# Optimization experiments

Hardware: AMD Instinct MI355X
Metric: run time of the kernel (lower is better)

Reference implementation:

```python
import jax, jax.numpy as jnp
import numpy as np
from jax import lax

FEAT_STRIDE = 16
NMS_THRESH = 0.7
N_PRE = 6000   # test-mode n_test_pre_nms
N_POST = 300   # test-mode n_test_post_nms
MIN_SIZE = 16.0
SCALE = 1.0
RATIOS = (0.5, 1.0, 2.0)
ANCHOR_SCALES = (8, 16, 32)
BASE = 16
N_ANCHOR = len(RATIOS) * len(ANCHOR_SCALES)  # 9


def _anchor_base():
    py = px = BASE / 2.0
    ab = np.zeros((N_ANCHOR, 4), np.float32)
    for i, r in enumerate(RATIOS):
        for j, s in enumerate(ANCHOR_SCALES):
            h = BASE * s * np.sqrt(r)
            w = BASE * s * np.sqrt(1.0 / r)
            k = i * len(ANCHOR_SCALES) + j
            ab[k] = [py - h / 2.0, px - w / 2.0, py + h / 2.0, px + w / 2.0]
    return ab


def _anchors(hh, ww):
    # enumerate_shifted_anchor: (y1,x1,y2,x2) anchors for every feature cell
    ab = _anchor_base()
    sy = np.arange(0, hh * FEAT_STRIDE, FEAT_STRIDE)
    sx = np.arange(0, ww * FEAT_STRIDE, FEAT_STRIDE)
    SX, SY = np.meshgrid(sx, sy)
    shift = np.stack([SY.ravel(), SX.ravel(), SY.ravel(), SX.ravel()], 1)
    anc = (ab[None, :, :] + shift[:, None, :]).reshape(-1, 4).astype(np.float32)
    return jnp.asarray(anc)


def _iou(b):
    # b: [N,4] (y1,x1,y2,x2) -> [N,N] IoU
    y1, x1, y2, x2 = b[:, 0], b[:, 1], b[:, 2], b[:, 3]
    area = (y2 - y1) * (x2 - x1)
    ih = jnp.clip(jnp.minimum(y2[:, None], y2[None, :]) - jnp.maximum(y1[:, None], y1[None, :]), 0.0)
    iw = jnp.clip(jnp.minimum(x2[:, None], x2[None, :]) - jnp.maximum(x1[:, None], x1[None, :]), 0.0)
    inter = ih * iw
    return inter / (area[:, None] + area[None, :] - inter + 1e-9)


def _propose(loc, fg, anchor, img_h, img_w):
    # loc:[M,4] fg:[M] anchor:[M,4]  -> padded [N_POST,4] rois + valid mask
    ah = anchor[:, 2] - anchor[:, 0]
    aw = anchor[:, 3] - anchor[:, 1]
    acy = anchor[:, 0] + 0.5 * ah
    acx = anchor[:, 1] + 0.5 * aw
    cy = loc[:, 0] * ah + acy
    cx = loc[:, 1] * aw + acx
    h = jnp.exp(loc[:, 2]) * ah
    w = jnp.exp(loc[:, 3]) * aw
    roi = jnp.stack([
        jnp.clip(cy - 0.5 * h, 0.0, img_h),
        jnp.clip(cx - 0.5 * w, 0.0, img_w),
        jnp.clip(cy + 0.5 * h, 0.0, img_h),
        jnp.clip(cx + 0.5 * w, 0.0, img_w),
    ], axis=1)
    hs = roi[:, 2] - roi[:, 0]
    ws = roi[:, 3] - roi[:, 1]
    ms = MIN_SIZE * SCALE
    valid = (hs >= ms) & (ws >= ms)
    sc = jnp.where(valid, fg, -jnp.inf)  # drop too-small boxes from ranking
    top_sc, idx = lax.top_k(sc, N_PRE)   # score-sorted pre-NMS candidates
    boxes = roi[idx]
    ok = lax.stop_gradient(jnp.isfinite(top_sc))
    sup = lax.stop_gradient(_iou(boxes) > NMS_THRESH)  # [N_PRE,N_PRE]
    tri = jnp.arange(N_PRE)

    def body(i, keep):
        suppressed = jnp.any(keep & sup[:, i] & (tri < i))
        return keep.at[i].set(ok[i] & ~suppressed)

    keep = lax.fori_loop(0, N_PRE, body, jnp.zeros((N_PRE,), bool))
    rank = jnp.cumsum(keep.astype(jnp.int32)) - 1
    sel = keep & (rank < N_POST)
    tgt = jnp.where(sel, rank, N_POST)  # N_POST is out-of-bounds -> dropped
    out = jnp.zeros((N_POST, 4), boxes.dtype).at[tgt].set(boxes, mode='drop')
    vmask = jnp.zeros((N_POST,), bool).at[tgt].set(True, mode='drop')
    return out, vmask


def reference(x, conv1_w, conv1_b, score_w, score_b, loc_w, loc_b, img_h, img_w):
    n, _, hh, ww = x.shape
    anchor = _anchors(hh, ww)
    h = jax.nn.relu(
        lax.conv_general_dilated(x, conv1_w, (1, 1), 'SAME',
                                 dimension_numbers=('NCHW', 'OIHW', 'NCHW'))
        + conv1_b[None, :, None, None])
    locs = jnp.einsum('nchw,oc->nohw', h, loc_w[:, :, 0, 0]) + loc_b[None, :, None, None]
    scr = jnp.einsum('nchw,oc->nohw', h, score_w[:, :, 0, 0]) + score_b[None, :, None, None]
    rpn_locs = locs.transpose(0, 2, 3, 1).reshape(n, -1, 4)          # [n,M,4]
    scr_t = scr.transpose(0, 2, 3, 1)                                 # [n,hh,ww,2A]
    soft = jax.nn.softmax(scr_t.reshape(n, hh, ww, N_ANCHOR, 2), axis=-1)
    fg = soft[..., 1].reshape(n, -1)                                  # [n,M]
    rpn_scores = scr_t.reshape(n, -1, 2)
    rois, vmask = jax.vmap(lambda l, f: _propose(l, f, anchor, img_h, img_w))(rpn_locs, fg)
    roi_indices = jnp.broadcast_to(jnp.arange(n, dtype=jnp.int32)[:, None], (n, N_POST))
    return rpn_locs, rpn_scores, rois, roi_indices, anchor, vmask


def setup_inputs() -> dict:
    key = jax.random.key(0)
    ks = jax.random.split(key, 4)
    x = jax.random.normal(ks[0], (2, 512, 64, 64), jnp.float32)
    conv1_w = 0.01 * jax.random.normal(ks[1], (512, 512, 3, 3), jnp.float32)
    conv1_b = jnp.zeros((512,), jnp.float32)
    score_w = 0.01 * jax.random.normal(ks[2], (N_ANCHOR * 2, 512, 1, 1), jnp.float32)
    score_b = jnp.zeros((N_ANCHOR * 2,), jnp.float32)
    loc_w = 0.01 * jax.random.normal(ks[3], (N_ANCHOR * 4, 512, 1, 1), jnp.float32)
    loc_b = jnp.zeros((N_ANCHOR * 4,), jnp.float32)
    return {"x": x, "conv1_w": conv1_w, "conv1_b": conv1_b,
            "score_w": score_w, "score_b": score_b,
            "loc_w": loc_w, "loc_b": loc_b,
            "img_h": 1024, "img_w": 1024}
```

## Files before the change

### kernel.cpp

```cpp
#include <hip/hip_runtime.h>
#include <hip/hip_bf16.h>
#include <math.h>
#include <cstdint>

typedef unsigned long long u64;
typedef unsigned int u32;
typedef _Float16 half8 __attribute__((ext_vector_type(8)));
typedef float floatx4 __attribute__((ext_vector_type(4)));

#define NANCH 36864
#define SEG 65536
#define N_PRE 6000
#define N_POST 300
#define NW 96
#define NPADC 6144
#define CAP 8192

#define O0 0
#define O1 294912
#define O2 442368
#define O3 444768
#define O4 445368
#define O5 592824

#define WS_XHI   0
#define WS_XLO   2097152
#define WS_WHI   4194304
#define WS_WLO   5373952
#define WS_WSLT  6553600
#define WS_WSLB  6586368
#define WS_H     6586432
#define WS_GUARD 10780736
#define WS_FG    0
#define WS_ROI   73728
#define WS_KEYS  368640
#define WS_SBOX  630784
#define WS_ALIVE 679936
#define WS_HIST  713088
#define WS_MASK  4194304

#define HSCALE 9.5367431640625e-07f

__device__ __forceinline__ void gl_lds16(const void* g, void* l) {
  __builtin_amdgcn_global_load_lds(
      (const __attribute__((address_space(1))) u32*)g,
      (__attribute__((address_space(3))) u32*)l, 16, 0, 0);
}

__device__ __forceinline__ u64 bcast64(u64 v, int src) {
  u32 lo = (u32)__shfl((int)(v & 0xFFFFFFFFull), src);
  u32 hi = (u32)__shfl((int)(v >> 32), src);
  return ((u64)hi << 32) | lo;
}

__device__ __forceinline__ int SWZ(int i) {
  return (i & ~15) | ((i ^ (i >> 4) ^ (i >> 8) ^ (i >> 12)) & 15);
}
__device__ __forceinline__ int SCX(int t) { return t + (t >> 5); }

__global__ __launch_bounds__(256) void prep_all(
    const float* __restrict__ x, const float* __restrict__ w,
    const float* __restrict__ lw, const float* __restrict__ sw,
    const float* __restrict__ lb, const float* __restrict__ sb,
    float4* __restrict__ h, float4* __restrict__ guard,
    _Float16* __restrict__ xhi, _Float16* __restrict__ xlo,
    _Float16* __restrict__ whi, _Float16* __restrict__ wlo,
    float* __restrict__ wslt, float* __restrict__ wslb) {
  __shared__ float s[64 * 65];
  const int b = blockIdx.x, tid = threadIdx.x;
  if (b < 4097) {
    int idx = b * 256 + tid;
    if (idx < 1048576) h[idx] = make_float4(0.f, 0.f, 0.f, 0.f);
    else if (idx < 1048576 + 16) guard[idx - 1048576] = make_float4(0.f, 0.f, 0.f, 0.f);
    return;
  }
  if (b < 5121) {
    int l = b - 4097;
    int pt = l & 63, cg = (l >> 6) & 7, n = l >> 9;
    const int c0 = cg << 6, p0 = pt << 6;
#pragma unroll
    for (int kk = 0; kk < 16; ++kk) {
      int e = tid + (kk << 8);
      int ci = e >> 6, pi = e & 63;
      s[ci * 65 + pi] = x[(((size_t)(n * 512 + c0 + ci)) << 12) + p0 + pi];
    }
    __syncthreads();
#pragma unroll
    for (int kk = 0; kk < 16; ++kk) {
      int e = tid + (kk << 8);
      int ci = e & 63, pi = e >> 6;
      float sv = s[ci * 65 + pi] * 1024.f;
      _Float16 hi = (_Float16)sv;
      _Float16 lo = (_Float16)(sv - (float)hi);
      size_t off = (((size_t)(n << 12) + p0 + pi) << 9) + c0 + ci;
      xhi[off] = hi;
      xlo[off] = lo;
    }
    return;
  }
  if (b < 5697) {
    int l = b - 5121;
    int ct = l & 7, ot = (l >> 3) & 7, t = l >> 6;
    const int c0 = ct << 6, o0 = ot << 6;
#pragma unroll
    for (int kk = 0; kk < 16; ++kk) {
      int e = tid + (kk << 8);
      int ci = e & 63, oi = e >> 6;
      float sv = w[(size_t)(o0 + oi) * 4608 + (c0 + ci) * 9 + t] * 1024.f;
      _Float16 hi = (_Float16)sv;
      _Float16 lo = (_Float16)(sv - (float)hi);
      size_t off = ((size_t)((t << 9) + o0 + oi) << 9) + c0 + ci;
      whi[off] = hi;
      wlo[off] = lo;
    }
    return;
  }
  {
    int e = (b - 5697) * 256 + tid;
    if (e < 32768) {
      int c = e >> 6, o = e & 63;
      float v = 0.f;
      if (o < 36) v = lw[o * 512 + c];
      else if (o < 54) v = sw[(o - 36) * 512 + c];
      wslt[e] = v;
    } else if (e < 32832) {
      int o = e - 32768;
      float v = 0.f;
      if (o < 36) v = lb[o];
      else if (o < 54) v = sb[o - 36];
      wslb[o] = v;
    }
  }
}

__global__ __launch_bounds__(256) void conv_mfma(
    const _Float16* __restrict__ xhi, const _Float16* __restrict__ xlo,
    const _Float16* __restrict__ whi, const _Float16* __restrict__ wlo,
    const float* __restrict__ guard, float* __restrict__ hout) {
  __shared__ _Float16 aHi[4 * 68 * 32];
  __shared__ _Float16 aLo[4 * 68 * 32];
  __shared__ _Float16 bHi[128 * 32];
  __shared__ _Float16 bLo[128 * 32];
  const int tid = threadIdx.x;
  const int lane = tid & 63, w = tid >> 6;
  const int ptile = blockIdx.x;
  const int og = blockIdx.y;
  const int kq = blockIdx.z;
  const int n = ptile >> 5;
  const int y0 = (ptile & 31) << 1;
  const int o0 = og << 7;
  const int l15 = lane & 15, l16 = lane >> 4;
  const int ry = w >> 1;
  const int wo = (w & 1) << 6;

  floatx4 acc[4][4];
#pragma unroll
  for (int a = 0; a < 4; ++a)
#pragma unroll
    for (int b = 0; b < 4; ++b) acc[a][b] = (floatx4)0.f;

  for (int s = 0; s < 8; ++s) {
    const int c0 = (kq << 8) + (s << 5);
    __syncthreads();
    for (int i = w; i < 17; i += 4) {
      int chunk = (i << 6) + lane;
      int p = chunk >> 2, q = chunk & 3;
      int r = p / 68, xs = p - r * 68;
      int y = y0 - 1 + r, xg = xs - 1;
      bool ok = ((unsigned)y < 64u) && ((unsigned)xg < 64u);
      size_t off = (((size_t)(n << 12) + (y << 6) + xg) << 9) + c0 + (q << 3);
      const void* gh = ok ? (const void*)(xhi + off) : (const void*)guard;
      const void* gl = ok ? (const void*)(xlo + off) : (const void*)guard;
      gl_lds16(gh, (char*)aHi + (i << 10));
      gl_lds16(gl, (char*)aLo + (i << 10));
    }
    for (int tt = 0; tt < 9; ++tt) {
      if (tt > 0) __syncthreads();
      for (int i = w; i < 8; i += 4) {
        int chunk = (i << 6) + lane;
        int row = chunk >> 2, q = chunk & 3;
        size_t off = ((size_t)((tt << 9) + o0 + row) << 9) + c0 + (q << 3);
        gl_lds16((const void*)(whi + off), (char*)bHi + (i << 10));
        gl_lds16((const void*)(wlo + off), (char*)bLo + (i << 10));
      }
      __syncthreads();

      const int dy = tt / 3, dx = tt - 3 * dy;
      half8 ah[4], al[4], bh[4], bl[4];
#pragma unroll
      for (int im = 0; im < 4; ++im) {
        int xp = (im << 4) + l15;
        int p = (ry + dy) * 68 + xp + dx;
        ah[im] = *(const half8*)&aHi[(p << 5) + (l16 << 3)];
        al[im] = *(const half8*)&aLo[(p << 5) + (l16 << 3)];
      }
#pragma unroll
      for (int in = 0; in < 4; ++in) {
        int orow = wo + (in << 4) + l15;
        bh[in] = *(const half8*)&bHi[(orow << 5) + (l16 << 3)];
        bl[in] = *(const half8*)&bLo[(orow << 5) + (l16 << 3)];
      }
#pragma unroll
      for (int im = 0; im < 4; ++im)
#pragma unroll
        for (int in = 0; in < 4; ++in) {
          acc[im][in] = __builtin_amdgcn_mfma_f32_16x16x32_f16(
              ah[im], bh[in], acc[im][in], 0, 0, 0);
          acc[im][in] = __builtin_amdgcn_mfma_f32_16x16x32_f16(
              ah[im], bl[in], acc[im][in], 0, 0, 0);
          acc[im][in] = __builtin_amdgcn_mfma_f32_16x16x32_f16(
              al[im], bh[in], acc[im][in], 0, 0, 0);
        }
    }
  }

#pragma unroll
  for (int im = 0; im < 4; ++im)
#pragma unroll
    for (int in = 0; in < 4; ++in) {
      int o = o0 + wo + (in << 4) + l15;
#pragma unroll
      for (int reg = 0; reg < 4; ++reg) {
        int m_local = (ry << 6) + (im << 4) + (l16 << 2) + reg;
        size_t off = (((size_t)(n << 12) + (y0 << 6) + m_local) << 9) + o;
        atomicAdd(&hout[off], acc[im][in][reg]);
      }
    }
}

__global__ __launch_bounds__(256) void head_kernel(
    const float* __restrict__ hbuf, const float* __restrict__ cb,
    const float* __restrict__ wslt, const float* __restrict__ wslb,
    float* __restrict__ out, float* __restrict__ fgbuf,
    uint4* __restrict__ hist4) {
  const int y = blockIdx.x, n = blockIdx.y, xq = blockIdx.z;
  __shared__ float sH[16 * 17];
  __shared__ float sWt[1024];
  __shared__ float sOut[64 * 17];
  const int tid = threadIdx.x;
  const int x4 = tid & 15, og = tid >> 4;
  const int x0 = xq << 4;

  if (xq == 0) {
    int gid = ((n << 6) + y) * 256 + tid;
    hist4[gid] = make_uint4(0u, 0u, 0u, 0u);
  }

  float acc[4];
#pragma unroll
  for (int j = 0; j < 4; ++j) acc[j] = 0.f;

  const float* hb = hbuf + (((size_t)(n << 12) + (y << 6) + x0) << 9);

  for (int c0 = 0; c0 < 512; c0 += 16) {
    __syncthreads();
    {
      int cc = tid & 15, xx = tid >> 4;
      float raw = hb[((size_t)xx << 9) + c0 + cc];
      sH[cc * 17 + xx] = fmaxf(raw * HSCALE + cb[c0 + cc], 0.f);
    }
#pragma unroll
    for (int p = 0; p < 4; ++p) {
      int e = tid + (p << 8);
      int cc = e >> 6, xx = e & 63;
      sWt[e] = wslt[((c0 + cc) << 6) + xx];
    }
    __syncthreads();
#pragma unroll
    for (int cc = 0; cc < 16; ++cc) {
      float hv = sH[cc * 17 + x4];
      float4 w0 = *(const float4*)&sWt[(cc << 6) + (og << 2)];
      acc[0] = fmaf(hv, w0.x, acc[0]);
      acc[1] = fmaf(hv, w0.y, acc[1]);
      acc[2] = fmaf(hv, w0.z, acc[2]);
      acc[3] = fmaf(hv, w0.w, acc[3]);
    }
  }
  __syncthreads();
#pragma unroll
  for (int j = 0; j < 4; ++j) {
    int o = (og << 2) + j;
    sOut[o * 17 + x4] = acc[j] + wslb[o];
  }
  __syncthreads();

  const int p0 = (n << 12) + (y << 6);
  float* locs = out + O0 + (size_t)p0 * 36 + (size_t)x0 * 36;
  for (int e = tid; e < 576; e += 256) {
    int xx = e / 36, o = e - xx * 36;
    locs[e] = sOut[o * 17 + xx];
  }
  float* scrs = out + O1 + (size_t)p0 * 18 + (size_t)x0 * 18;
  for (int e = tid; e < 288; e += 256) {
    int xx = e / 18, ss = e - xx * 18;
    scrs[e] = sOut[(36 + ss) * 17 + xx];
  }
  float* fg = fgbuf + n * NANCH + ((y << 6) + x0) * 9;
  for (int e = tid; e < 144; e += 256) {
    int xx = e / 9, a = e - xx * 9;
    float s0 = sOut[(36 + 2 * a) * 17 + xx];
    float s1 = sOut[(36 + 2 * a + 1) * 17 + xx];
    fg[e] = 1.0f / (1.0f + expf(s0 - s1));
  }
}

__global__ __launch_bounds__(256) void decode_kernel(
    const float* __restrict__ out0, const float* __restrict__ fgbuf,
    float4* __restrict__ roibuf, u64* __restrict__ keys,
    float* __restrict__ anchor_out, float* __restrict__ out,
    u32* __restrict__ hist,
    const int* __restrict__ imgh_p, const int* __restrict__ imgw_p) {
  int gid = blockIdx.x * 256 + threadIdx.x;
  if (gid < 3600) {
    if (gid < 2400) out[O2 + gid] = 0.f;
    else if (gid < 3000) out[O3 + (gid - 2400)] = (float)((gid - 2400) / 300);
    else out[O5 + (gid - 3000)] = 0.f;
  }
  int n = gid >> 16, k = gid & (SEG - 1);
  if (k >= NANCH) return;
  int a = k % 9;
  int p = k / 9;
  int py = p >> 6, px = p & 63;

  const double R[3] = {0.5, 1.0, 2.0};
  const double S[3] = {8.0, 16.0, 32.0};
  double r = R[a / 3], s = S[a - (a / 3) * 3];
  double hd = 16.0 * s * sqrt(r);
  double wd = 16.0 * s * sqrt(1.0 / r);
  float ay1 = (float)(8.0 - hd / 2.0) + (float)(py * 16);
  float ax1 = (float)(8.0 - wd / 2.0) + (float)(px * 16);
  float ay2 = (float)(8.0 + hd / 2.0) + (float)(py * 16);
  float ax2 = (float)(8.0 + wd / 2.0) + (float)(px * 16);
  if (n == 0) {
    float* ao = anchor_out + (size_t)k * 4;
    ao[0] = ay1; ao[1] = ax1; ao[2] = ay2; ao[3] = ax2;
  }
  float ahk = ay2 - ay1, awk = ax2 - ax1;
  float acy = ay1 + 0.5f * ahk, acx = ax1 + 0.5f * awk;
  const float* lp = out0 + ((size_t)(n * NANCH + k) << 2);
  float dy = lp[0], dx = lp[1], dh = lp[2], dw = lp[3];
  float cy = dy * ahk + acy;
  float cx = dx * awk + acx;
  float bh = expf(dh) * ahk;
  float bw = expf(dw) * awk;
  float img_h = (float)imgh_p[0], img_w = (float)imgw_p[0];
  float y1 = fminf(fmaxf(cy - 0.5f * bh, 0.f), img_h);
  float x1 = fminf(fmaxf(cx - 0.5f * bw, 0.f), img_w);
  float y2 = fminf(fmaxf(cy + 0.5f * bh, 0.f), img_h);
  float x2 = fminf(fmaxf(cx + 0.5f * bw, 0.f), img_w);
  bool valid = ((y2 - y1) >= 16.f) && ((x2 - x1) >= 16.f);
  float sc = valid ? fgbuf[n * NANCH + k] : -INFINITY;
  roibuf[n * NANCH + k] = make_float4(y1, x1, y2, x2);
  unsigned int b = __float_as_uint(sc);
  unsigned int m = b ^ ((b & 0x80000000u) ? 0xFFFFFFFFu : 0x80000000u);
  u32 hk = ~m;
  keys[gid] = ((u64)hk << 32) | (unsigned int)k;
  if (hk < 0xFF800000u) atomicAdd(&hist[(n << 16) + (hk >> 16)], 1u);
}

__global__ __launch_bounds__(1024) void select_kernel(
    const u32* __restrict__ hist, const u64* __restrict__ keys,
    const float4* __restrict__ roibuf,
    float4* __restrict__ sbox, u64* __restrict__ alive) {
  __shared__ u64 sk[CAP];
  __shared__ u32 sT, sCnt;
  u32* sc = (u32*)sk;
  const int n = blockIdx.x, t = threadIdx.x;

  const uint4* hp = (const uint4*)(hist + (n << 16));
  u32 s = 0;
#pragma unroll
  for (int q = 0; q < 16; ++q) {
    uint4 v = hp[t * 16 + q];
    s += v.x + v.y + v.z + v.w;
  }
  if (t == 0) { sT = 0u; sCnt = 0u; }
  sc[SCX(t)] = s;
  __syncthreads();
  for (int off = 1; off < 1024; off <<= 1) {
    u32 v = (t >= off) ? sc[SCX(t - off)] : 0u;
    __syncthreads();
    sc[SCX(t)] += v;
    __syncthreads();
  }
  u32 total = sc[SCX(1023)];
  u32 target = total < (u32)N_PRE ? total : (u32)N_PRE;
  u32 mycum = sc[SCX(t)];
  u32 prev = t ? sc[SCX(t - 1)] : 0u;
  __syncthreads();
  if (total > 0 && mycum >= target && prev < target) {
    u32 base = prev;
    int b = t << 6;
    while (true) {
      base += hist[(n << 16) + b];
      if (base >= target) break;
      ++b;
    }
    sT = (u32)b;
  }
  __syncthreads();
  const u32 T = sT;
  const bool any = (total > 0);

  for (int e = t; e < CAP; e += 1024) sk[e] = ~0ull;
  __syncthreads();
  const u64 below = (t & 63) ? (~0ull >> (64 - (t & 63))) : 0ull;
  for (int i = t; i < NANCH; i += 1024) {
    u64 key = keys[(n << 16) + i];
    u32 hk = (u32)(key >> 32);
    bool take = any && hk < 0xFF800000u && (hk >> 16) <= T;
    u64 bal = __ballot(take);
    u32 base = 0;
    if ((t & 63) == 0 && bal) base = atomicAdd(&sCnt, (u32)__popcll(bal));
    base = (u32)__shfl((int)base, 0);
    if (take) {
      u32 slot = base + (u32)__popcll(bal & below);
      if (slot < (u32)CAP) sk[SWZ(slot)] = key;
    }
  }
  __syncthreads();

  for (int k = 2; k <= CAP; k <<= 1) {
    for (int j = k >> 1; j > 0; j >>= 1) {
      for (int q = t; q < (CAP >> 1); q += 1024) {
        int l = ((q & ~(j - 1)) << 1) | (q & (j - 1));
        int rr = l | j;
        bool asc = ((l & k) == 0);
        int pl = SWZ(l), pr = SWZ(rr);
        u64 a = sk[pl], b = sk[pr];
        if ((a > b) == asc) { sk[pl] = b; sk[pr] = a; }
      }
      __syncthreads();
    }
  }

  for (int i = t; i < NPADC; i += 1024) {
    u64 kk = sk[SWZ(i)];
    bool valid = (i < N_PRE) && ((u32)(kk >> 32) < 0xFF800000u);
    float4 b = make_float4(0.f, 0.f, 0.f, 0.f);
    if (valid) b = roibuf[(size_t)n * NANCH + (u32)(kk & 0xFFFFFFFFull)];
    sbox[n * NPADC + i] = b;
    u64 bal = __ballot(valid);
    if ((t & 63) == 0) alive[n * NW + (i >> 6)] = bal;
  }
}

__global__ __launch_bounds__(256) void build_mask(
    const float4* __restrict__ sbox, u64* __restrict__ M) {
  __shared__ float4 jb[4][64];
  __shared__ float ja[4][64];
  const int tid = threadIdx.x, lane = tid & 63, wv = tid >> 6;
  const int g = blockIdx.x, q = blockIdx.y, n = blockIdx.z;
  const float4* sb = sbox + n * NPADC;
  float4 bi = sb[(g << 6) + lane];
  float ai = (bi.z - bi.x) * (bi.w - bi.y);
  u64* Mrow = M + ((size_t)(n * NPADC + (g << 6) + lane)) * NW;
#pragma unroll
  for (int it = 0; it < 6; ++it) {
    int w = q * 24 + (it << 2) + wv;
    if (w < g) continue;
    float4 bjl = sb[(w << 6) + lane];
    jb[wv][lane] = bjl;
    ja[wv][lane] = (bjl.z - bjl.x) * (bjl.w - bjl.y);
    u64 bits = 0;
#pragma unroll 8
    for (int j = 0; j < 64; ++j) {
      float4 bj = jb[wv][j];
      float aj = ja[wv][j];
      float ih = fmaxf(fminf(bi.z, bj.z) - fmaxf(bi.x, bj.x), 0.f);
      float iw = fmaxf(fminf(bi.w, bj.w) - fmaxf(bi.y, bj.y), 0.f);
      float inter = ih * iw;
      bool bit = inter / (ai + aj - inter + 1e-9f) > 0.7f;
      bits |= ((u64)bit) << j;
    }
    Mrow[w] = bits;
  }
}

__global__ __launch_bounds__(64) void nms_reduce(
    const u64* __restrict__ M, const u64* __restrict__ alive,
    const float4* __restrict__ sbox, float* __restrict__ out) {
  const int n = blockIdx.x, lane = threadIdx.x;
  float* rois = out + O2 + n * (N_POST * 4);
  float* vmask = out + O5 + n * N_POST;
  const u64* A = alive + n * NW;
  const u64* Mb = M + (size_t)n * NPADC * NW;
  const float4* sb = sbox + n * NPADC;
  u64 aw0 = A[lane];
  u64 aw1 = (lane < 32) ? A[64 + lane] : 0ull;
  u64 accA = 0, accB = 0;
  int nk = 0;
  u64 dnext = Mb[(size_t)lane * NW + 0];
  float4 bnext = sb[lane];
  const u64 below = lane ? (~0ull >> (64 - lane)) : 0ull;

  for (int c = 0; c < 94; ++c) {
    u64 dcur = dnext;
    float4 bcur = bnext;
    if (c + 1 < 94) {
      dnext = Mb[(size_t)(((c + 1) << 6) + lane) * NW + (c + 1)];
      bnext = sb[((c + 1) << 6) + lane];
    }
    u64 wacc = (c < 64) ? bcast64(accA, c) : bcast64(accB, c - 64);
    u64 aw = (c < 64) ? bcast64(aw0, c) : bcast64(aw1, c - 64);
    u64 alive_u = aw & ~wacc;
    if (alive_u == 0ull) continue;

    u64 dmask = dcur & below;
    u64 rem = alive_u, kept = 0;
    while (rem) {
      int j = __builtin_ctzll(rem);
      kept |= 1ull << j;
      u64 col = __ballot((dmask >> j) & 1);
      rem &= ~(col | (1ull << j));
    }

    int npop = __popcll(kept);
    if ((kept >> lane) & 1ull) {
      int slot = nk + __popcll(kept & below);
      if (slot < N_POST) {
        rois[slot * 4 + 0] = bcur.x; rois[slot * 4 + 1] = bcur.y;
        rois[slot * 4 + 2] = bcur.z; rois[slot * 4 + 3] = bcur.w;
        vmask[slot] = 1.0f;
      }
    }
    if (nk + npop >= N_POST) break;
    nk += npop;

    u64 kk = kept;
    while (kk) {
      int j0 = __builtin_ctzll(kk); kk &= kk - 1;
      int j1 = kk ? __builtin_ctzll(kk) : j0; kk &= kk - 1;
      int j2 = kk ? __builtin_ctzll(kk) : j0; kk &= kk - 1;
      int j3 = kk ? __builtin_ctzll(kk) : j0; kk &= kk - 1;
      int j4 = kk ? __builtin_ctzll(kk) : j0; kk &= kk - 1;
      int j5 = kk ? __builtin_ctzll(kk) : j0; kk &= kk - 1;
      int j6 = kk ? __builtin_ctzll(kk) : j0; kk &= kk - 1;
      int j7 = kk ? __builtin_ctzll(kk) : j0; kk &= kk - 1;
      const u64* r0 = Mb + (size_t)((c << 6) + j0) * NW;
      const u64* r1 = Mb + (size_t)((c << 6) + j1) * NW;
      const u64* r2 = Mb + (size_t)((c << 6) + j2) * NW;
      const u64* r3 = Mb + (size_t)((c << 6) + j3) * NW;
      const u64* r4 = Mb + (size_t)((c << 6) + j4) * NW;
      const u64* r5 = Mb + (size_t)((c << 6) + j5) * NW;
      const u64* r6 = Mb + (size_t)((c << 6) + j6) * NW;
      const u64* r7 = Mb + (size_t)((c << 6) + j7) * NW;
      u64 oA = r0[lane] | r1[lane] | r2[lane] | r3[lane]
             | r4[lane] | r5[lane] | r6[lane] | r7[lane];
      u64 oB = 0;
      if (lane < 32)
        oB = r0[64 + lane] | r1[64 + lane] | r2[64 + lane] | r3[64 + lane]
           | r4[64 + lane] | r5[64 + lane] | r6[64 + lane] | r7[64 + lane];
      accA |= oA;
      accB |= oB;
    }
  }
}

extern "C" void kernel_launch(void* const* d_in, const int* in_sizes, int n_in,
                              void* d_out, int out_size, void* d_ws, size_t ws_size,
                              hipStream_t stream) {
  const float* x        = (const float*)d_in[0];
  const float* conv1_w  = (const float*)d_in[1];
  const float* conv1_b  = (const float*)d_in[2];
  const float* score_w  = (const float*)d_in[3];
  const float* score_b  = (const float*)d_in[4];
  const float* loc_w    = (const float*)d_in[5];
  const float* loc_b    = (const float*)d_in[6];
  const int*   imgh_p   = (const int*)d_in[7];
  const int*   imgw_p   = (const int*)d_in[8];

  float* out = (float*)d_out;
  float* ws  = (float*)d_ws;

  _Float16* xhi = (_Float16*)(ws + WS_XHI);
  _Float16* xlo = (_Float16*)(ws + WS_XLO);
  _Float16* whi = (_Float16*)(ws + WS_WHI);
  _Float16* wlo = (_Float16*)(ws + WS_WLO);
  float* wslt   = ws + WS_WSLT;
  float* wslb   = ws + WS_WSLB;
  float* hbuf   = ws + WS_H;
  float* guard  = ws + WS_GUARD;
  float* fgbuf   = ws + WS_FG;
  float4* roibuf = (float4*)(ws + WS_ROI);
  u64* keys      = (u64*)(ws + WS_KEYS);
  float4* sbox   = (float4*)(ws + WS_SBOX);
  u64* alive     = (u64*)(ws + WS_ALIVE);
  u32* hist      = (u32*)(ws + WS_HIST);
  u64* maskbuf   = (u64*)(ws + WS_MASK);

  prep_all<<<5826, 256, 0, stream>>>(x, conv1_w, loc_w, score_w, loc_b, score_b,
                                     (float4*)hbuf, (float4*)guard,
                                     xhi, xlo, whi, wlo, wslt, wslb);

  conv_mfma<<<dim3(64, 4, 2), 256, 0, stream>>>(xhi, xlo, whi, wlo, guard, hbuf);

  head_kernel<<<dim3(64, 2, 4), 256, 0, stream>>>(hbuf, conv1_b, wslt, wslb, out,
                                                  fgbuf, (uint4*)hist);
  decode_kernel<<<512, 256, 0, stream>>>(out, fgbuf, roibuf, keys,
                                         out + O4, out, hist, imgh_p, imgw_p);

  select_kernel<<<2, 1024, 0, stream>>>(hist, keys, roibuf, sbox, alive);

  build_mask<<<dim3(96, 4, 2), 256, 0, stream>>>(sbox, maskbuf);
  nms_reduce<<<2, 64, 0, stream>>>(maskbuf, alive, sbox, out);
}
```

Baseline: 506.9 us.

## Replace single-block bitonic sort with parallel compaction and rank-by-count scatter

```diff
diff --git a/kernel.cpp b/kernel.cpp
--- a/kernel.cpp
+++ b/kernel.cpp
@@ -36,6 +36,7 @@
 #define WS_KEYS  368640
 #define WS_SBOX  630784
 #define WS_ALIVE 679936
+#define WS_CBUF  680320
 #define WS_HIST  713088
 #define WS_MASK  4194304
 
@@ -53,9 +54,6 @@
   return ((u64)hi << 32) | lo;
 }
 
-__device__ __forceinline__ int SWZ(int i) {
-  return (i & ~15) | ((i ^ (i >> 4) ^ (i >> 8) ^ (i >> 12)) & 15);
-}
 __device__ __forceinline__ int SCX(int t) { return t + (t >> 5); }
 
 __global__ __launch_bounds__(256) void prep_all(
@@ -308,9 +306,13 @@
     const float* __restrict__ out0, const float* __restrict__ fgbuf,
     float4* __restrict__ roibuf, u64* __restrict__ keys,
     float* __restrict__ anchor_out, float* __restrict__ out,
-    u32* __restrict__ hist,
+    u32* __restrict__ hist, u64* __restrict__ cbuf,
+    float4* __restrict__ sbox, u64* __restrict__ alive,
     const int* __restrict__ imgh_p, const int* __restrict__ imgw_p) {
   int gid = blockIdx.x * 256 + threadIdx.x;
+  if (gid < 16384) cbuf[gid] = ~0ull;
+  if (gid < 12288) sbox[gid] = make_float4(0.f, 0.f, 0.f, 0.f);
+  if (gid < 192) alive[gid] = 0ull;
   if (gid < 3600) {
     if (gid < 2400) out[O2 + gid] = 0.f;
     else if (gid < 3000) out[O3 + (gid - 2400)] = (float)((gid - 2400) / 300);
@@ -358,13 +360,11 @@
   if (hk < 0xFF800000u) atomicAdd(&hist[(n << 16) + (hk >> 16)], 1u);
 }
 
-__global__ __launch_bounds__(1024) void select_kernel(
+__global__ __launch_bounds__(1024) void compact_kernel(
     const u32* __restrict__ hist, const u64* __restrict__ keys,
-    const float4* __restrict__ roibuf,
-    float4* __restrict__ sbox, u64* __restrict__ alive) {
-  __shared__ u64 sk[CAP];
+    u64* __restrict__ cbuf) {
+  __shared__ u32 sc[1064];
   __shared__ u32 sT, sCnt;
-  u32* sc = (u32*)sk;
   const int n = blockIdx.x, t = threadIdx.x;
 
   const uint4* hp = (const uint4*)(hist + (n << 16));
@@ -387,7 +387,6 @@
   u32 target = total < (u32)N_PRE ? total : (u32)N_PRE;
   u32 mycum = sc[SCX(t)];
   u32 prev = t ? sc[SCX(t - 1)] : 0u;
-  __syncthreads();
   if (total > 0 && mycum >= target && prev < target) {
     u32 base = prev;
     int b = t << 6;
@@ -402,8 +401,6 @@
   const u32 T = sT;
   const bool any = (total > 0);
 
-  for (int e = t; e < CAP; e += 1024) sk[e] = ~0ull;
-  __syncthreads();
   const u64 below = (t & 63) ? (~0ull >> (64 - (t & 63))) : 0ull;
   for (int i = t; i < NANCH; i += 1024) {
     u64 key = keys[(n << 16) + i];
@@ -415,33 +412,33 @@
     base = (u32)__shfl((int)base, 0);
     if (take) {
       u32 slot = base + (u32)__popcll(bal & below);
-      if (slot < (u32)CAP) sk[SWZ(slot)] = key;
-    }
-  }
-  __syncthreads();
-
-  for (int k = 2; k <= CAP; k <<= 1) {
-    for (int j = k >> 1; j > 0; j >>= 1) {
-      for (int q = t; q < (CAP >> 1); q += 1024) {
-        int l = ((q & ~(j - 1)) << 1) | (q & (j - 1));
-        int rr = l | j;
-        bool asc = ((l & k) == 0);
-        int pl = SWZ(l), pr = SWZ(rr);
-        u64 a = sk[pl], b = sk[pr];
-        if ((a > b) == asc) { sk[pl] = b; sk[pr] = a; }
-      }
-      __syncthreads();
-    }
-  }
-
-  for (int i = t; i < NPADC; i += 1024) {
-    u64 kk = sk[SWZ(i)];
-    bool valid = (i < N_PRE) && ((u32)(kk >> 32) < 0xFF800000u);
-    float4 b = make_float4(0.f, 0.f, 0.f, 0.f);
-    if (valid) b = roibuf[(size_t)n * NANCH + (u32)(kk & 0xFFFFFFFFull)];
-    sbox[n * NPADC + i] = b;
-    u64 bal = __ballot(valid);
-    if ((t & 63) == 0) alive[n * NW + (i >> 6)] = bal;
+      if (slot < (u32)CAP) cbuf[(n << 13) + slot] = key;
+    }
+  }
+}
+
+#define RTILE 512
+__global__ __launch_bounds__(256) void rank_scatter(
+    const u64* __restrict__ cbuf, const float4* __restrict__ roibuf,
+    float4* __restrict__ sbox, u64* __restrict__ alive) {
+  __shared__ u64 lk[RTILE];
+  const int n = blockIdx.y;
+  const int i = blockIdx.x * 256 + threadIdx.x;
+  const u64* cb = cbuf + (n << 13);
+  const u64 mykey = cb[i];
+  u32 rank = 0;
+  for (int t0 = 0; t0 < CAP; t0 += RTILE) {
+    __syncthreads();
+    lk[threadIdx.x] = cb[t0 + threadIdx.x];
+    lk[256 + threadIdx.x] = cb[t0 + 256 + threadIdx.x];
+    __syncthreads();
+#pragma unroll 8
+    for (int j = 0; j < RTILE; ++j) rank += (lk[j] < mykey) ? 1u : 0u;
+  }
+  if (mykey != ~0ull && rank < (u32)N_PRE) {
+    u32 k = (u32)(mykey & 0xFFFFFFFFull);
+    sbox[n * NPADC + rank] = roibuf[(size_t)n * NANCH + k];
+    atomicOr(&alive[n * NW + (rank >> 6)], 1ull << (rank & 63));
   }
 }
 
@@ -586,6 +583,7 @@
   u64* keys      = (u64*)(ws + WS_KEYS);
   float4* sbox   = (float4*)(ws + WS_SBOX);
   u64* alive     = (u64*)(ws + WS_ALIVE);
+  u64* cbuf      = (u64*)(ws + WS_CBUF);
   u32* hist      = (u32*)(ws + WS_HIST);
   u64* maskbuf   = (u64*)(ws + WS_MASK);
 
@@ -598,9 +596,11 @@
   head_kernel<<<dim3(64, 2, 4), 256, 0, stream>>>(hbuf, conv1_b, wslt, wslb, out,
                                                   fgbuf, (uint4*)hist);
   decode_kernel<<<512, 256, 0, stream>>>(out, fgbuf, roibuf, keys,
-                                         out + O4, out, hist, imgh_p, imgw_p);
-
-  select_kernel<<<2, 1024, 0, stream>>>(hist, keys, roibuf, sbox, alive);
+                                         out + O4, out, hist, cbuf, sbox, alive,
+                                         imgh_p, imgw_p);
+
+  compact_kernel<<<2, 1024, 0, stream>>>(hist, keys, cbuf);
+  rank_scatter<<<dim3(32, 2), 256, 0, stream>>>(cbuf, roibuf, sbox, alive);
 
   build_mask<<<dim3(96, 4, 2), 256, 0, stream>>>(sbox, maskbuf);
   nms_reduce<<<2, 64, 0, stream>>>(maskbuf, alive, sbox, out);
```

New measurement: 532.4 us. 5.0% more time.
